# Optimization experiments

Hardware: AMD Instinct MI355X
Metric: run time of the kernel (lower is better)

## Reference

```python
import jax, jax.numpy as jnp
import numpy as np

B, S, D, T = 64, 1024, 768, 10
IS = int(S * 0.3)   # 307, token-mix inner dim
ID = int(D * 0.3)   # 230, channel-mix inner dim
EPS = 1e-5


def _cond_ln(x, embed, tid):
    # LayerNorm over last dim (no affine), then per-sample gamma/beta
    mu = jnp.mean(x, axis=-1, keepdims=True)
    var = jnp.mean(jnp.square(x - mu), axis=-1, keepdims=True)
    out = (x - mu) / jnp.sqrt(var + EPS)
    gb = embed[tid]                      # [B, 2D]
    gamma, beta = gb[:, :D], gb[:, D:]
    return gamma[:, None, :] * out + beta[:, None, :]


def setup_inputs() -> dict:
    key = jax.random.key(0)
    ks = jax.random.split(key, 8)
    x = jax.random.normal(ks[0], (B, S, D), dtype=jnp.float32)
    tasks_id = jax.random.randint(ks[1], (B,), 0, T)
    # conditional LN embeddings: gamma ~ N(1, 0.02), beta = 0
    cln1 = jnp.concatenate([1.0 + 0.02 * jax.random.normal(ks[2], (T, D)),
                            jnp.zeros((T, D))], axis=1).astype(jnp.float32)
    cln2 = jnp.concatenate([1.0 + 0.02 * jax.random.normal(ks[3], (T, D)),
                            jnp.zeros((T, D))], axis=1).astype(jnp.float32)
    # per-task weights stored [T, fout, fin] (kaiming-ish scale)
    w1_tok = jax.random.normal(ks[4], (T, IS, S), dtype=jnp.float32) * (2.0 / S) ** 0.5
    w2_tok = jax.random.normal(ks[5], (T, S, IS), dtype=jnp.float32) * (2.0 / IS) ** 0.5
    w1_ch = jax.random.normal(ks[6], (T, ID, D), dtype=jnp.float32) * (2.0 / D) ** 0.5
    w2_ch = jax.random.normal(ks[7], (T, D, ID), dtype=jnp.float32) * (2.0 / ID) ** 0.5
    return {"x": x, "tasks_id": tasks_id, "cln1": cln1, "cln2": cln2,
            "w1_tok": w1_tok, "w2_tok": w2_tok, "w1_ch": w1_ch, "w2_ch": w2_ch}


def reference(x, tasks_id, cln1, cln2, w1_tok, w2_tok, w1_ch, w2_ch):
    tid = tasks_id
    # --- token-mixing block (axis=1 ConditionalLinear) ---
    h = _cond_ln(x, cln1, tid)
    h = jnp.einsum('bnd,bcn->bcd', h, w1_tok[tid])   # [B, IS, D]
    h = jax.nn.gelu(h, approximate=False)
    h = jnp.einsum('bnd,bcn->bcd', h, w2_tok[tid])   # [B, S, D]
    x = x + h
    # --- channel-mixing block (axis=2 ConditionalLinear) ---
    h = _cond_ln(x, cln2, tid)
    h = jnp.einsum('bnd,bcd->bnc', h, w1_ch[tid])    # [B, S, ID]
    h = jax.nn.gelu(h, approximate=False)
    h = jnp.einsum('bnd,bcd->bnc', h, w2_ch[tid])    # [B, S, D]
    x = x + h
    return x
```

## Files before the change

kernel.cpp:

```cpp
#include <hip/hip_runtime.h>
#include <math.h>

typedef __bf16 bf16x8 __attribute__((ext_vector_type(8)));
typedef __bf16 bf16x4 __attribute__((ext_vector_type(4)));
typedef float  f32x4  __attribute__((ext_vector_type(4)));

constexpr int Bc = 64, Sc = 1024, Dc = 768;
constexpr int ISc = 307, IDc = 230;
constexpr int ISp = 384, IDp = 256;

static __device__ __forceinline__ float bf2f(unsigned short u) {
    return __builtin_bit_cast(float, (unsigned)u << 16);
}
static __device__ __forceinline__ float gelu_f(float v) {
    return 0.5f * v * (1.0f + erff(v * 0.70710678118654752f));
}

static __device__ __forceinline__ void gload16(const void* g, void* l) {
    __builtin_amdgcn_global_load_lds(
        (const __attribute__((address_space(1))) void*)g,
        (__attribute__((address_space(3))) void*)l, 16, 0, 0);
}

constexpr int CH0 = 10 * ISp * (Sc  / 8);
constexpr int CH1 = 10 * Sc  * (ISp / 8);
constexpr int CH2 = 10 * IDp * (Dc  / 8);
constexpr int CH3 = 10 * Dc  * (IDp / 8);
constexpr int CB0 = CH0, CB1 = CB0 + CH1, CB2 = CB1 + CH2, CB3 = CB2 + CH3;

__device__ __forceinline__ void cvt_one(
    const float* __restrict__ in, __bf16* __restrict__ out,
    int inrows, int outrows, int incols, int outcols, int c)
{
    const int cpr  = outcols >> 3;
    const int perT = outrows * cpr;
    const int t    = c / perT;
    const int rem  = c - t * perT;
    const int r    = rem / cpr;
    const int cc   = (rem - r * cpr) * 8;
    bf16x8 o;
    if (r < inrows) {
        const float* src = in + ((long)t * inrows + r) * incols + cc;
        #pragma unroll
        for (int e = 0; e < 8; e++)
            o[e] = (cc + e < incols) ? (__bf16)src[e] : (__bf16)0.0f;
    } else {
        #pragma unroll
        for (int e = 0; e < 8; e++) o[e] = (__bf16)0.0f;
    }
    *reinterpret_cast<bf16x8*>(out + ((long)t * outrows + r) * outcols + cc) = o;
}

__global__ __launch_bounds__(256) void cvt_all(
    const float* __restrict__ w1t, const float* __restrict__ w2t,
    const float* __restrict__ w1c, const float* __restrict__ w2c,
    __bf16* __restrict__ o1t, __bf16* __restrict__ o2t,
    __bf16* __restrict__ o1c, __bf16* __restrict__ o2c)
{
    const int c = blockIdx.x * 256 + threadIdx.x;
    if (c < CB0)      cvt_one(w1t, o1t, ISc, ISp, Sc,  Sc,  c);
    else if (c < CB1) cvt_one(w2t, o2t, Sc,  Sc,  ISc, ISp, c - CB0);
    else if (c < CB2) cvt_one(w1c, o1c, IDc, IDp, Dc,  Dc,  c - CB1);
    else if (c < CB3) cvt_one(w2c, o2c, Dc,  Dc,  IDc, IDp, c - CB2);
}

__global__ __launch_bounds__(256) void ln1_t(
    const float* __restrict__ x, const int* __restrict__ tasks,
    const float* __restrict__ cln, __bf16* __restrict__ h1T)
{
    constexpr int RPB = 32, LDT = Dc + 8;
    __shared__ unsigned short T[RPB * LDT];
    const int b   = blockIdx.y;
    const int t   = tasks[b];
    const int s0  = blockIdx.x * RPB;
    const int tid = threadIdx.x;
    const int wv  = tid >> 6;
    const int l   = tid & 63;

    const float4* Ga = reinterpret_cast<const float4*>(cln + (long)t * 2 * Dc);
    const float4* Be = reinterpret_cast<const float4*>(cln + (long)t * 2 * Dc + Dc);
    const float4 g0 = Ga[l], g1 = Ga[l + 64], g2 = Ga[l + 128];
    const float4 b0 = Be[l], b1 = Be[l + 64], b2 = Be[l + 128];

    #pragma unroll
    for (int rr = 0; rr < 8; rr++) {
        const int r = wv * 8 + rr;
        const float4* xr = reinterpret_cast<const float4*>(x + ((long)b * Sc + s0 + r) * Dc);
        const float4 v0 = xr[l], v1 = xr[l + 64], v2 = xr[l + 128];
        float s = v0.x + v0.y + v0.z + v0.w + v1.x + v1.y + v1.z + v1.w
                + v2.x + v2.y + v2.z + v2.w;
        float q = v0.x*v0.x + v0.y*v0.y + v0.z*v0.z + v0.w*v0.w
                + v1.x*v1.x + v1.y*v1.y + v1.z*v1.z + v1.w*v1.w
                + v2.x*v2.x + v2.y*v2.y + v2.z*v2.z + v2.w*v2.w;
        #pragma unroll
        for (int o = 1; o < 64; o <<= 1) { s += __shfl_xor(s, o); q += __shfl_xor(q, o); }
        const float mu   = s * (1.0f / Dc);
        const float var  = fmaxf(q * (1.0f / Dc) - mu * mu, 0.0f);
        const float rstd = 1.0f / sqrtf(var + 1e-5f);
        unsigned short* tr = &T[r * LDT];
        bf16x4 o0, o1, o2;
        o0[0] = (__bf16)(g0.x * ((v0.x - mu) * rstd) + b0.x);
        o0[1] = (__bf16)(g0.y * ((v0.y - mu) * rstd) + b0.y);
        o0[2] = (__bf16)(g0.z * ((v0.z - mu) * rstd) + b0.z);
        o0[3] = (__bf16)(g0.w * ((v0.w - mu) * rstd) + b0.w);
        o1[0] = (__bf16)(g1.x * ((v1.x - mu) * rstd) + b1.x);
        o1[1] = (__bf16)(g1.y * ((v1.y - mu) * rstd) + b1.y);
        o1[2] = (__bf16)(g1.z * ((v1.z - mu) * rstd) + b1.z);
        o1[3] = (__bf16)(g1.w * ((v1.w - mu) * rstd) + b1.w);
        o2[0] = (__bf16)(g2.x * ((v2.x - mu) * rstd) + b2.x);
        o2[1] = (__bf16)(g2.y * ((v2.y - mu) * rstd) + b2.y);
        o2[2] = (__bf16)(g2.z * ((v2.z - mu) * rstd) + b2.z);
        o2[3] = (__bf16)(g2.w * ((v2.w - mu) * rstd) + b2.w);
        *reinterpret_cast<bf16x4*>(&tr[l * 4])        = o0;
        *reinterpret_cast<bf16x4*>(&tr[256 + l * 4])  = o1;
        *reinterpret_cast<bf16x4*>(&tr[512 + l * 4])  = o2;
    }
    __syncthreads();
    #pragma unroll
    for (int c = 0; c < 3; c++) {
        const int d = tid + c * 256;
        unsigned short tmp[32];
        #pragma unroll
        for (int e = 0; e < 32; e++) tmp[e] = T[e * LDT + d];
        __bf16* dst = h1T + ((long)b * Dc + d) * Sc + s0;
        #pragma unroll
        for (int u = 0; u < 4; u++)
            reinterpret_cast<uint4*>(dst)[u] = reinterpret_cast<const uint4*>(tmp)[u];
    }
}

template<int DOGELU, int RESM, int OUTF32, int ATASK>
__global__ __launch_bounds__(256, 2) void gemm_tn(
    const __bf16* __restrict__ A, long sA, int lda,
    const __bf16* __restrict__ B, long sB, int ldb,
    const void* __restrict__ R, long sR,
    void* __restrict__ C, long sC, int ldc,
    const int* __restrict__ tasks, int M, int N, int K)
{
    constexpr int BM = 128, BN = 128, BK = 64;
    constexpr int BUFB = 32768;
    __shared__ uint4 lds4[2 * BUFB / 16];
    char* lbase = (char*)lds4;

    const int gx  = gridDim.x, gy = gridDim.y;
    const int tpb = gx * gy;
    const long lin = blockIdx.x + (long)gx * (blockIdx.y + (long)gy * blockIdx.z);
    const int  xcd  = (int)(lin & 7);
    const long idx  = lin >> 3;
    const int  lb   = (int)(idx / tpb);
    const int  tile = (int)(idx - (long)lb * tpb);
    const int  b    = xcd * 8 + lb;
    const int  m0   = (tile / gx) * BM;
    const int  n0   = (tile % gx) * BN;

    const int t = tasks[b];
    const __bf16* Ab = A + (ATASK ? (long)t : (long)b) * sA;
    const __bf16* Bb = B + (ATASK ? (long)b : (long)t) * sB;
    const int tid = threadIdx.x, lane = tid & 63, wid = tid >> 6;
    const int wm = (wid >> 1) * 64, wn = (wid & 1) * 64;
    const int l15 = lane & 15, l4 = lane >> 4;

    f32x4 acc[4][4];
    #pragma unroll
    for (int i = 0; i < 4; i++)
        #pragma unroll
        for (int j = 0; j < 4; j++)
            acc[i][j] = (f32x4){0.f, 0.f, 0.f, 0.f};

    auto STAGE = [&](int k0, int buf) {
        char* dst = lbase + buf * BUFB;
        #pragma unroll
        for (int rep = 0; rep < 4; rep++) {
            const int c = rep * 256 + tid;
            const int m = c >> 3, ch = c & 7;
            const int gk = k0 + ((ch ^ (m & 7)) << 3);
            gload16(Ab + (long)(m0 + m) * lda + gk, dst + c * 16);
        }
        #pragma unroll
        for (int rep = 0; rep < 4; rep++) {
            const int c = rep * 256 + tid;
            const int n = c >> 3, ch = c & 7;
            const int gk = k0 + ((ch ^ (n & 7)) << 3);
            gload16(Bb + (long)(n0 + n) * ldb + gk, dst + 16384 + c * 16);
        }
    };

    const int nt = K / BK;
    STAGE(0, 0);
    __syncthreads();
    int cur = 0;
    for (int tt = 0; tt < nt; tt++) {
        if (tt + 1 < nt) STAGE((tt + 1) * BK, cur ^ 1);
        const char* bb = lbase + cur * BUFB;
        #pragma unroll
        for (int h = 0; h < 2; h++) {
            bf16x8 af[4], bfr[4];
            #pragma unroll
            for (int i = 0; i < 4; i++) {
                const int row = wm + i * 16 + l15;
                af[i] = *reinterpret_cast<const bf16x8*>(
                    bb + row * 128 + (((h * 4 + l4) ^ (row & 7)) << 4));
            }
            #pragma unroll
            for (int j = 0; j < 4; j++) {
                const int row = wn + j * 16 + l15;
                bfr[j] = *reinterpret_cast<const bf16x8*>(
                    bb + 16384 + row * 128 + (((h * 4 + l4) ^ (row & 7)) << 4));
            }
            #pragma unroll
            for (int i = 0; i < 4; i++)
                #pragma unroll
                for (int j = 0; j < 4; j++)
                    acc[i][j] = __builtin_amdgcn_mfma_f32_16x16x32_bf16(af[i], bfr[j], acc[i][j], 0, 0, 0);
        }
        __syncthreads();
        cur ^= 1;
    }

    float*  Cf = (float*)C  + (long)b * sC;
    __bf16* Ch = (__bf16*)C + (long)b * sC;
    const float*  Rf = (RESM == 1) ? ((const float*)R  + (long)b * sR) : nullptr;
    const __bf16* Rh = (RESM == 2) ? ((const __bf16*)R + (long)b * sR) : nullptr;

    #pragma unroll
    for (int i = 0; i < 4; i++) {
        #pragma unroll
        for (int j = 0; j < 4; j++) {
            const int gn = n0 + wn + j * 16 + l15;
            #pragma unroll
            for (int r = 0; r < 4; r++) {
                const int gm = m0 + wm + i * 16 + l4 * 4 + r;
                float v = acc[i][j][r];
                if (DOGELU) v = gelu_f(v);
                if (RESM == 1) v += Rf[(long)gm * ldc + gn];
                if (RESM == 2) v += (float)Rh[(long)gm * ldc + gn];
                if (OUTF32) Cf[(long)gm * ldc + gn] = v;
                else        Ch[(long)gm * ldc + gn] = (__bf16)v;
            }
        }
    }
}

__global__ __launch_bounds__(512, 1) void mlp_ch(
    const __bf16* __restrict__ x1, const int* __restrict__ tasks,
    const float* __restrict__ cln2,
    const __bf16* __restrict__ wC1,
    const __bf16* __restrict__ wC2,
    float* __restrict__ out)
{
    __shared__ float2 st[128];
    __shared__ unsigned short G[128 * 256];
    __shared__ char sbuf[2][32768];

    const int lin = blockIdx.x;
    const int xcd = lin & 7;
    const int idx = lin >> 3;
    const int b   = xcd * 8 + (idx >> 3);
    const int m0  = (idx & 7) * 128;
    const int t   = tasks[b];

    const int tid = threadIdx.x;
    const int wid = tid >> 6, lane = tid & 63;
    const int g   = wid >> 2, wid2 = wid & 3;
    const int wm  = (wid2 >> 1) * 64, wn = (wid2 & 1) * 64;
    const int l15 = lane & 15, l4 = lane >> 4;

    const __bf16* xb = x1 + ((long)b * Sc + m0) * Dc;
    const float*  cg = cln2 + (long)t * 2 * Dc;
    const float*  cb = cg + Dc;

    #pragma unroll 2
    for (int rr = 0; rr < 16; rr++) {
        const int m = wid * 16 + rr;
        const ushort4* xr = reinterpret_cast<const ushort4*>(xb + (long)m * Dc);
        const ushort4 u0 = xr[lane], u1 = xr[lane + 64], u2 = xr[lane + 128];
        float s = 0.f, q = 0.f, v;
        v = bf2f(u0.x); s += v; q += v*v;  v = bf2f(u0.y); s += v; q += v*v;
        v = bf2f(u0.z); s += v; q += v*v;  v = bf2f(u0.w); s += v; q += v*v;
        v = bf2f(u1.x); s += v; q += v*v;  v = bf2f(u1.y); s += v; q += v*v;
        v = bf2f(u1.z); s += v; q += v*v;  v = bf2f(u1.w); s += v; q += v*v;
        v = bf2f(u2.x); s += v; q += v*v;  v = bf2f(u2.y); s += v; q += v*v;
        v = bf2f(u2.z); s += v; q += v*v;  v = bf2f(u2.w); s += v; q += v*v;
        #pragma unroll
        for (int o = 1; o < 64; o <<= 1) { s += __shfl_xor(s, o); q += __shfl_xor(q, o); }
        if (lane == 0) {
            const float mu  = s * (1.0f / Dc);
            const float var = fmaxf(q * (1.0f / Dc) - mu * mu, 0.0f);
            st[m] = make_float2(mu, 1.0f / sqrtf(var + 1e-5f));
        }
    }
    __syncthreads();

    const int am = tid >> 2, ach = tid & 3;
    const float2 ams = st[am];
    const __bf16* arow = xb + (long)am * Dc;

    auto loadA = [&](int kt) -> bf16x8 {
        return *reinterpret_cast<const bf16x8*>(arow + kt * 32 + ach * 8);
    };
    auto writeA = [&](bf16x8 a, int buf) {
        const int gk = 0;  (void)gk;
        *reinterpret_cast<bf16x8*>(sbuf[buf] + am * 64 + ((ach ^ (am & 3)) << 4)) = a;
    };
    auto stageB1 = [&](int kt, int buf) {
        #pragma unroll
        for (int rep = 0; rep < 2; rep++) {
            const int c = rep * 512 + tid;
            const int n = c >> 2, ch = c & 3;
            const int gk = kt * 32 + ((ch ^ (n & 3)) << 3);
            gload16(wC1 + ((long)t * IDp + n) * Dc + gk, sbuf[buf] + 8192 + c * 16);
        }
    };
    auto xformA = [&](bf16x8 raw, int kt) -> bf16x8 {
        const int gk = kt * 32 + ach * 8;
        const float4 ga0 = reinterpret_cast<const float4*>(cg + gk)[0];
        const float4 ga1 = reinterpret_cast<const float4*>(cg + gk)[1];
        const float4 be0 = reinterpret_cast<const float4*>(cb + gk)[0];
        const float4 be1 = reinterpret_cast<const float4*>(cb + gk)[1];
        bf16x8 o;
        o[0] = (__bf16)(ga0.x * ((float)raw[0] - ams.x) * ams.y + be0.x);
        o[1] = (__bf16)(ga0.y * ((float)raw[1] - ams.x) * ams.y + be0.y);
        o[2] = (__bf16)(ga0.z * ((float)raw[2] - ams.x) * ams.y + be0.z);
        o[3] = (__bf16)(ga0.w * ((float)raw[3] - ams.x) * ams.y + be0.w);
        o[4] = (__bf16)(ga1.x * ((float)raw[4] - ams.x) * ams.y + be1.x);
        o[5] = (__bf16)(ga1.y * ((float)raw[5] - ams.x) * ams.y + be1.y);
        o[6] = (__bf16)(ga1.z * ((float)raw[6] - ams.x) * ams.y + be1.z);
        o[7] = (__bf16)(ga1.w * ((float)raw[7] - ams.x) * ams.y + be1.w);
        return o;
    };

    f32x4 acc[4][4];
    #pragma unroll
    for (int i = 0; i < 4; i++)
        #pragma unroll
        for (int j = 0; j < 4; j++)
            acc[i][j] = (f32x4){0.f, 0.f, 0.f, 0.f};

    {
        bf16x8 a0 = loadA(0);
        stageB1(0, 0);
        writeA(xformA(a0, 0), 0);
        __syncthreads();
        for (int kt = 0; kt < 24; kt++) {
            const int buf = kt & 1;
            bf16x8 anx;
            if (kt < 23) { anx = loadA(kt + 1); stageB1(kt + 1, buf ^ 1); }
            const char* Abase = sbuf[buf];
            const char* Bbase = sbuf[buf] + 8192;
            bf16x8 af[4], bfr[4];
            #pragma unroll
            for (int i = 0; i < 4; i++) {
                const int row = wm + i * 16 + l15;
                af[i] = *reinterpret_cast<const bf16x8*>(
                    Abase + row * 64 + ((l4 ^ (row & 3)) << 4));
            }
            #pragma unroll
            for (int j = 0; j < 4; j++) {
                const int row = g * 128 + wn + j * 16 + l15;
                bfr[j] = *reinterpret_cast<const bf16x8*>(
                    Bbase + row * 64 + ((l4 ^ (row & 3)) << 4));
            }
            #pragma unroll
            for (int i = 0; i < 4; i++)
                #pragma unroll
                for (int j = 0; j < 4; j++)
                    acc[i][j] = __builtin_amdgcn_mfma_f32_16x16x32_bf16(af[i], bfr[j], acc[i][j], 0, 0, 0);
            if (kt < 23) writeA(xformA(anx, kt + 1), buf ^ 1);
            __syncthreads();
        }
    }

    #pragma unroll
    for (int i = 0; i < 4; i++) {
        #pragma unroll
        for (int j = 0; j < 4; j++) {
            const int k = g * 128 + wn + j * 16 + l15;
            #pragma unroll
            for (int r = 0; r < 4; r++) {
                const int m = wm + i * 16 + l4 * 4 + r;
                const float v = gelu_f(acc[i][j][r]);
                const int chunk = k >> 3;
                const int phys  = chunk ^ (m & 7);
                G[m * 256 + phys * 8 + (k & 7)] =
                    __builtin_bit_cast(unsigned short, (__bf16)v);
            }
        }
    }
    __syncthreads();

    const __bf16* w2b = wC2 + (long)t * Dc * IDp;
    for (int nc = 0; nc < 3; nc++) {
        auto stageB2 = [&](int kt, int buf) {
            #pragma unroll
            for (int rep = 0; rep < 4; rep++) {
                const int c = rep * 512 + tid;
                const int n = c >> 3, ch = c & 7;
                const int gk = kt * 64 + ((ch ^ (n & 7)) << 3);
                gload16(w2b + (long)(nc * 256 + n) * IDp + gk, sbuf[buf] + c * 16);
            }
        };
        f32x4 a2[4][4];
        #pragma unroll
        for (int i = 0; i < 4; i++)
            #pragma unroll
            for (int j = 0; j < 4; j++)
                a2[i][j] = (f32x4){0.f, 0.f, 0.f, 0.f};

        stageB2(0, 0);
        __syncthreads();
        for (int kt = 0; kt < 4; kt++) {
            const int buf = kt & 1;
            if (kt < 3) stageB2(kt + 1, buf ^ 1);
            #pragma unroll
            for (int h = 0; h < 2; h++) {
                bf16x8 af[4], bfr[4];
                #pragma unroll
                for (int i = 0; i < 4; i++) {
                    const int row = wm + i * 16 + l15;
                    const int chunk = kt * 8 + h * 4 + l4;
                    const int phys  = chunk ^ (row & 7);
                    af[i] = *reinterpret_cast<const bf16x8*>(
                        (const char*)G + row * 512 + phys * 16);
                }
                #pragma unroll
                for (int j = 0; j < 4; j++) {
                    const int row = g * 128 + wn + j * 16 + l15;
                    bfr[j] = *reinterpret_cast<const bf16x8*>(
                        sbuf[buf] + row * 128 + (((h * 4 + l4) ^ (row & 7)) << 4));
                }
                #pragma unroll
                for (int i = 0; i < 4; i++)
                    #pragma unroll
                    for (int j = 0; j < 4; j++)
                        a2[i][j] = __builtin_amdgcn_mfma_f32_16x16x32_bf16(af[i], bfr[j], a2[i][j], 0, 0, 0);
            }
            __syncthreads();
        }
        float* ob = out + ((long)b * Sc + m0) * Dc;
        #pragma unroll
        for (int i = 0; i < 4; i++) {
            #pragma unroll
            for (int j = 0; j < 4; j++) {
                const int gn = nc * 256 + g * 128 + wn + j * 16 + l15;
                #pragma unroll
                for (int r = 0; r < 4; r++) {
                    const int gm = wm + i * 16 + l4 * 4 + r;
                    ob[(long)gm * Dc + gn] =
                        a2[i][j][r] + (float)xb[(long)gm * Dc + gn];
                }
            }
        }
    }
}

extern "C" void kernel_launch(void* const* d_in, const int* in_sizes, int n_in,
                              void* d_out, int out_size, void* d_ws, size_t ws_size,
                              hipStream_t stream) {
    const float* x      = (const float*)d_in[0];
    const int*   tasks  = (const int*)  d_in[1];
    const float* cln1   = (const float*)d_in[2];
    const float* cln2   = (const float*)d_in[3];
    const float* w1_tok = (const float*)d_in[4];
    const float* w2_tok = (const float*)d_in[5];
    const float* w1_ch  = (const float*)d_in[6];
    const float* w2_ch  = (const float*)d_in[7];
    float* out = (float*)d_out;

    char* ws = (char*)d_ws;
    const long oT1 = 0;
    const long oT2 = oT1 + (long)10 * ISp * Sc * 2;
    const long oC1 = oT2 + (long)10 * Sc * ISp * 2;
    const long oC2 = oC1 + (long)10 * IDp * Dc * 2;
    const long oA  = oC2 + (long)10 * Dc * IDp * 2;
    const long oG  = oA  + (long)Bc * Dc * Sc * 2;
    __bf16* wT1  = (__bf16*)(ws + oT1);
    __bf16* wT2  = (__bf16*)(ws + oT2);
    __bf16* wC1  = (__bf16*)(ws + oC1);
    __bf16* wC2  = (__bf16*)(ws + oC2);
    __bf16* h1T  = (__bf16*)(ws + oA);
    __bf16* x1   = (__bf16*)(ws + oA);
    __bf16* gbf  = (__bf16*)(ws + oG);

    const dim3 blk(256);
    auto cdiv = [](long a, long b) { return (int)((a + b - 1) / b); };

    cvt_all<<<cdiv(CB3, 256), blk, 0, stream>>>(
        w1_tok, w2_tok, w1_ch, w2_ch, wT1, wT2, wC1, wC2);

    ln1_t<<<dim3(Sc / 32, Bc), blk, 0, stream>>>(x, tasks, cln1, h1T);

    gemm_tn<1, 0, 0, 0><<<dim3(ISp / 128, Dc / 128, Bc), blk, 0, stream>>>(
        h1T, (long)Dc * Sc, Sc,
        wT1, (long)ISp * Sc, Sc,
        nullptr, 0,
        gbf, (long)Dc * ISp, ISp,
        tasks, Dc, ISp, Sc);

    gemm_tn<0, 1, 0, 1><<<dim3(Dc / 128, Sc / 128, Bc), blk, 0, stream>>>(
        wT2, (long)Sc * ISp, ISp,
        gbf, (long)Dc * ISp, ISp,
        x, (long)Sc * Dc,
        x1, (long)Sc * Dc, Dc,
        tasks, Sc, Dc, ISp);

    mlp_ch<<<(Sc / 128) * Bc, 512, 0, stream>>>(x1, tasks, cln2, wC1, wC2, out);
}
```

Baseline: 451.4 us.

## Shrink channel-MLP blocks to 64 rows and 256 threads for two blocks per CU

The fused channel-mixing kernel now processes 64 rows per block with 4 waves instead of 128 rows with 8 waves. Shared memory use drops so two blocks can be resident per CU, and the launch doubles the grid. The intent is better latency hiding and load balance from higher occupancy. In exchange, each block re-reads the full per-task weight tiles for half as many rows, which raises weight traffic. The second GEMM also moves to narrower 32-wide K tiles with more loop iterations and barriers.

```diff
diff --git a/kernel.cpp b/kernel.cpp
--- a/kernel.cpp
+++ b/kernel.cpp
@@ -241,28 +241,27 @@
     }
 }
 
-__global__ __launch_bounds__(512, 1) void mlp_ch(
+__global__ __launch_bounds__(256, 2) void mlp_ch(
     const __bf16* __restrict__ x1, const int* __restrict__ tasks,
     const float* __restrict__ cln2,
     const __bf16* __restrict__ wC1,
     const __bf16* __restrict__ wC2,
     float* __restrict__ out)
 {
-    __shared__ float2 st[128];
-    __shared__ unsigned short G[128 * 256];
-    __shared__ char sbuf[2][32768];
+    __shared__ float2 st[64];
+    __shared__ unsigned short G[64 * 256];
+    __shared__ char sbuf[2][20480];
 
     const int lin = blockIdx.x;
     const int xcd = lin & 7;
     const int idx = lin >> 3;
-    const int b   = xcd * 8 + (idx >> 3);
-    const int m0  = (idx & 7) * 128;
+    const int b   = xcd * 8 + (idx >> 4);
+    const int m0  = (idx & 15) * 64;
     const int t   = tasks[b];
 
     const int tid = threadIdx.x;
     const int wid = tid >> 6, lane = tid & 63;
-    const int g   = wid >> 2, wid2 = wid & 3;
-    const int wm  = (wid2 >> 1) * 64, wn = (wid2 & 1) * 64;
+    const int wn  = wid * 64;
     const int l15 = lane & 15, l4 = lane >> 4;
 
     const __bf16* xb = x1 + ((long)b * Sc + m0) * Dc;
@@ -299,16 +298,15 @@
         return *reinterpret_cast<const bf16x8*>(arow + kt * 32 + ach * 8);
     };
     auto writeA = [&](bf16x8 a, int buf) {
-        const int gk = 0;  (void)gk;
         *reinterpret_cast<bf16x8*>(sbuf[buf] + am * 64 + ((ach ^ (am & 3)) << 4)) = a;
     };
     auto stageB1 = [&](int kt, int buf) {
         #pragma unroll
-        for (int rep = 0; rep < 2; rep++) {
-            const int c = rep * 512 + tid;
+        for (int rep = 0; rep < 4; rep++) {
+            const int c = rep * 256 + tid;
             const int n = c >> 2, ch = c & 3;
             const int gk = kt * 32 + ((ch ^ (n & 3)) << 3);
-            gload16(wC1 + ((long)t * IDp + n) * Dc + gk, sbuf[buf] + 8192 + c * 16);
+            gload16(wC1 + ((long)t * IDp + n) * Dc + gk, sbuf[buf] + 4096 + c * 16);
         }
     };
     auto xformA = [&](bf16x8 raw, int kt) -> bf16x8 {
@@ -346,17 +344,17 @@
             bf16x8 anx;
             if (kt < 23) { anx = loadA(kt + 1); stageB1(kt + 1, buf ^ 1); }
             const char* Abase = sbuf[buf];
-            const char* Bbase = sbuf[buf] + 8192;
+            const char* Bbase = sbuf[buf] + 4096;
             bf16x8 af[4], bfr[4];
             #pragma unroll
             for (int i = 0; i < 4; i++) {
-                const int row = wm + i * 16 + l15;
+                const int row = i * 16 + l15;
                 af[i] = *reinterpret_cast<const bf16x8*>(
                     Abase + row * 64 + ((l4 ^ (row & 3)) << 4));
             }
             #pragma unroll
             for (int j = 0; j < 4; j++) {
-                const int row = g * 128 + wn + j * 16 + l15;
+                const int row = wn + j * 16 + l15;
                 bfr[j] = *reinterpret_cast<const bf16x8*>(
                     Bbase + row * 64 + ((l4 ^ (row & 3)) << 4));
             }
@@ -374,13 +372,12 @@
     for (int i = 0; i < 4; i++) {
         #pragma unroll
         for (int j = 0; j < 4; j++) {
-            const int k = g * 128 + wn + j * 16 + l15;
+            const int k = wn + j * 16 + l15;
             #pragma unroll
             for (int r = 0; r < 4; r++) {
-                const int m = wm + i * 16 + l4 * 4 + r;
+                const int m = i * 16 + l4 * 4 + r;
                 const float v = gelu_f(acc[i][j][r]);
-                const int chunk = k >> 3;
-                const int phys  = chunk ^ (m & 7);
+                const int phys = (k >> 3) ^ (m & 7);
                 G[m * 256 + phys * 8 + (k & 7)] =
                     __builtin_bit_cast(unsigned short, (__bf16)v);
             }
@@ -389,13 +386,14 @@
     __syncthreads();
 
     const __bf16* w2b = wC2 + (long)t * Dc * IDp;
+    float* ob = out + ((long)b * Sc + m0) * Dc;
     for (int nc = 0; nc < 3; nc++) {
         auto stageB2 = [&](int kt, int buf) {
             #pragma unroll
             for (int rep = 0; rep < 4; rep++) {
-                const int c = rep * 512 + tid;
-                const int n = c >> 3, ch = c & 7;
-                const int gk = kt * 64 + ((ch ^ (n & 7)) << 3);
+                const int c = rep * 256 + tid;
+                const int n = c >> 2, ch = c & 3;
+                const int gk = kt * 32 + ((ch ^ (n & 3)) << 3);
                 gload16(w2b + (long)(nc * 256 + n) * IDp + gk, sbuf[buf] + c * 16);
             }
         };
@@ -408,43 +406,38 @@
 
         stageB2(0, 0);
         __syncthreads();
-        for (int kt = 0; kt < 4; kt++) {
+        for (int kt = 0; kt < 8; kt++) {
             const int buf = kt & 1;
-            if (kt < 3) stageB2(kt + 1, buf ^ 1);
-            #pragma unroll
-            for (int h = 0; h < 2; h++) {
-                bf16x8 af[4], bfr[4];
+            if (kt < 7) stageB2(kt + 1, buf ^ 1);
+            bf16x8 af[4], bfr[4];
+            #pragma unroll
+            for (int i = 0; i < 4; i++) {
+                const int row = i * 16 + l15;
+                const int phys = (kt * 4 + l4) ^ (row & 7);
+                af[i] = *reinterpret_cast<const bf16x8*>(
+                    (const char*)G + row * 512 + phys * 16);
+            }
+            #pragma unroll
+            for (int j = 0; j < 4; j++) {
+                const int row = wn + j * 16 + l15;
+                bfr[j] = *reinterpret_cast<const bf16x8*>(
+                    sbuf[buf] + row * 64 + ((l4 ^ (row & 3)) << 4));
+            }
+            #pragma unroll
+            for (int i = 0; i < 4; i++)
                 #pragma unroll
-                for (int i = 0; i < 4; i++) {
-                    const int row = wm + i * 16 + l15;
-                    const int chunk = kt * 8 + h * 4 + l4;
-                    const int phys  = chunk ^ (row & 7);
-                    af[i] = *reinterpret_cast<const bf16x8*>(
-                        (const char*)G + row * 512 + phys * 16);
-                }
-                #pragma unroll
-                for (int j = 0; j < 4; j++) {
-                    const int row = g * 128 + wn + j * 16 + l15;
-                    bfr[j] = *reinterpret_cast<const bf16x8*>(
-                        sbuf[buf] + row * 128 + (((h * 4 + l4) ^ (row & 7)) << 4));
-                }
-                #pragma unroll
-                for (int i = 0; i < 4; i++)
-                    #pragma unroll
-                    for (int j = 0; j < 4; j++)
-                        a2[i][j] = __builtin_amdgcn_mfma_f32_16x16x32_bf16(af[i], bfr[j], a2[i][j], 0, 0, 0);
-            }
+                for (int j = 0; j < 4; j++)
+                    a2[i][j] = __builtin_amdgcn_mfma_f32_16x16x32_bf16(af[i], bfr[j], a2[i][j], 0, 0, 0);
             __syncthreads();
         }
-        float* ob = out + ((long)b * Sc + m0) * Dc;
         #pragma unroll
         for (int i = 0; i < 4; i++) {
             #pragma unroll
             for (int j = 0; j < 4; j++) {
-                const int gn = nc * 256 + g * 128 + wn + j * 16 + l15;
+                const int gn = nc * 256 + wn + j * 16 + l15;
                 #pragma unroll
                 for (int r = 0; r < 4; r++) {
-                    const int gm = wm + i * 16 + l4 * 4 + r;
+                    const int gm = i * 16 + l4 * 4 + r;
                     ob[(long)gm * Dc + gn] =
                         a2[i][j][r] + (float)xb[(long)gm * Dc + gn];
                 }
@@ -503,5 +496,5 @@
         x1, (long)Sc * Dc, Dc,
         tasks, Sc, Dc, ISp);
 
-    mlp_ch<<<(Sc / 128) * Bc, 512, 0, stream>>>(x1, tasks, cln2, wC1, wC2, out);
-}
+    mlp_ch<<<(Sc / 64) * Bc, blk, 0, stream>>>(x1, tasks, cln2, wC1, wC2, out);
+}
```

After: 453.1 us. Within noise of the previous version (+0.4%).
